# Kernel tuning notes

Hardware: AMD Instinct MI355X
Metric: run time of the kernel (lower is better)

## Reference

```python
import jax, jax.numpy as jnp
import numpy as np

BATCH, SEQ, DIM = 32, 1024, 256
CODEBOOK_SIZE = 8192
COMMITMENT_COST = 0.25
CODEBOOK_COST = 1.0


def setup_inputs() -> dict:
    key = jax.random.key(0)
    kx, kc = jax.random.split(key)
    x = jax.random.normal(kx, (BATCH, SEQ, DIM), dtype=jnp.float32)
    codebook = jax.random.normal(kc, (CODEBOOK_SIZE, DIM), dtype=jnp.float32)
    return {"x": x, "codebook": codebook, "hidden_dim": DIM}


def reference(x, codebook, hidden_dim):
    # x: [B, S, D], codebook: [K, D]
    B, S, D = x.shape
    flat = x.reshape(-1, D)  # [N, D], N = B*S
    distances = (
        jnp.sum(flat * flat, axis=1, keepdims=True)
        + jnp.sum(codebook * codebook, axis=1)
        - 2.0 * jnp.matmul(flat, codebook.T)
    )
    encoding_indices = jnp.argmin(distances, axis=1)  # [N]
    quantized = codebook[encoding_indices].reshape(x.shape)  # [B, S, D]
    # Losses (detach semantics only matter for gradients; value is same MSE)
    codebook_loss = jnp.mean((quantized - jax.lax.stop_gradient(x)) ** 2)
    commitment_loss = jnp.mean((jax.lax.stop_gradient(quantized) - x) ** 2)
    total_loss = CODEBOOK_COST * codebook_loss + COMMITMENT_COST * commitment_loss
    # Straight-through estimator
    quantized_ste = x + jax.lax.stop_gradient(quantized - x)
    return (quantized_ste, total_loss)
```

## Files before the change

kernel.cpp:

```cpp
#include <hip/hip_runtime.h>
#include <hip/hip_fp16.h>

#define NROWS 32768
#define DIMS 256
#define KCODES 8192
#define NH 2
#define HCODES 4096
#define MARGIN 0.10f

typedef _Float16 half8 __attribute__((ext_vector_type(8)));
typedef float f32x4 __attribute__((ext_vector_type(4)));
typedef unsigned long long u64;

__device__ __forceinline__ void gload_lds16(const void* g, void* l) {
  __builtin_amdgcn_global_load_lds((const __attribute__((address_space(1))) unsigned int*)g,
                                   (__attribute__((address_space(3))) unsigned int*)l, 16, 0, 0);
}

__device__ __forceinline__ unsigned sortable_f32(float f) {
  unsigned u = __float_as_uint(f);
  return u ^ (unsigned)(((int)u >> 31) | 0x80000000);
}
__device__ __forceinline__ float unsortable_f32(unsigned s) {
  const unsigned m = ((int)s < 0) ? 0x80000000u : 0xFFFFFFFFu;
  return __uint_as_float(s ^ m);
}
__device__ __forceinline__ u64 umin64(u64 a, u64 b) { return a < b ? a : b; }
__device__ __forceinline__ u64 umax64(u64 a, u64 b) { return a > b ? a : b; }
__device__ __forceinline__ float dkey(u64 k) { return unsortable_f32((unsigned)(k >> 32)); }

__global__ void k_prep(const float* __restrict__ cb, _Float16* __restrict__ cbh) {
  const int g = blockIdx.x * 256 + threadIdx.x;
  const float4 v0 = *((const float4*)cb + g * 2);
  const float4 v1 = *((const float4*)cb + g * 2 + 1);
  half8 h;
  h[0] = (_Float16)v0.x; h[1] = (_Float16)v0.y;
  h[2] = (_Float16)v0.z; h[3] = (_Float16)v0.w;
  h[4] = (_Float16)v1.x; h[5] = (_Float16)v1.y;
  h[6] = (_Float16)v1.z; h[7] = (_Float16)v1.w;
  *((half8*)cbh + g) = h;
}

__global__ void k_cnorm(const float* __restrict__ cb, float* __restrict__ cnorm,
                        int* __restrict__ wcount, int* __restrict__ scount,
                        float* __restrict__ loss_cell) {
  const int lane = threadIdx.x & 63;
  const int code = blockIdx.x * 4 + (threadIdx.x >> 6);
  const float4 v = *((const float4*)(cb + code * DIMS) + lane);
  float s = v.x * v.x + v.y * v.y + v.z * v.z + v.w * v.w;
#pragma unroll
  for (int m = 1; m < 64; m <<= 1) s += __shfl_xor(s, m);
  if (lane == 0) cnorm[code] = s;
  if (blockIdx.x == 0 && threadIdx.x == 0) {
    *wcount = 0; *scount = 0; *loss_cell = 0.0f;
  }
}

__launch_bounds__(512)
__global__ void k_gemm2(const float* __restrict__ x, const _Float16* __restrict__ cbh,
                        const float* __restrict__ cnorm,
                        u64* __restrict__ pk1, u64* __restrict__ pk2,
                        float* __restrict__ d3h) {
  __shared__ char B[2][32768];
  const int tid = threadIdx.x;
  const int lane = tid & 63;
  const int w = tid >> 6;
  const int l15 = lane & 15;
  const int lh = lane >> 4;
  const int rowblk = (int)blockIdx.x >> 1;
  const int half = (int)blockIdx.x & 1;
  const int row0 = rowblk * 256 + w * 32;
  const char* cbh_half = (const char*)(cbh + (size_t)half * HCODES * DIMS);

  half8 a[2][8];
#pragma unroll
  for (int m = 0; m < 2; ++m) {
#pragma unroll
    for (int kf = 0; kf < 8; ++kf) {
      const float* s = x + (size_t)(row0 + m * 16 + l15) * DIMS + kf * 32 + lh * 8;
      const float4 v0 = *(const float4*)s;
      const float4 v1 = *(const float4*)(s + 4);
      half8 h;
      h[0] = (_Float16)v0.x; h[1] = (_Float16)v0.y;
      h[2] = (_Float16)v0.z; h[3] = (_Float16)v0.w;
      h[4] = (_Float16)v1.x; h[5] = (_Float16)v1.y;
      h[6] = (_Float16)v1.z; h[7] = (_Float16)v1.w;
      a[m][kf] = h;
    }
  }

  int srcoff[4];
#pragma unroll
  for (int i = 0; i < 4; ++i) {
    const int L = i * 512 + tid;
    const int hi = L >> 6;
    const int lhL = hi & 3, chL = hi >> 2;
    const int code = (L & 63) ^ ((lhL & 1) << 4);
    srcoff[i] = code * 512 + chL * 64 + lhL * 16;
  }

  const int lanebase = l15 * 16 + lh * 1024;
  const int bs = (lh & 1) << 8;
  const int lbp = lanebase + bs;
  const int lbm = lanebase - bs;

  float r1[2][4], r2[2][4];
  int i1[2][4];
#pragma unroll
  for (int m = 0; m < 2; ++m)
#pragma unroll
    for (int j = 0; j < 4; ++j) { r1[m][j] = 3.0e38f; r2[m][j] = 3.0e38f; i1[m][j] = 0; }

  char* lds = &B[0][0];

  auto stage = [&](int t, int bufoff) {
#pragma unroll
    for (int i = 0; i < 4; ++i)
      gload_lds16(cbh_half + t * 32768 + srcoff[i],
                  lds + bufoff + (i * 512 + w * 64) * 16);
  };

  auto compute_tile = [&](int t, int bufoff) {
    const int cbase = half * HCODES + t * 64;
    float cn[4];
#pragma unroll
    for (int n = 0; n < 4; ++n) cn[n] = cnorm[cbase + n * 16 + l15];
    f32x4 acc[2][4];
#pragma unroll
    for (int m = 0; m < 2; ++m)
#pragma unroll
      for (int n = 0; n < 4; ++n) acc[m][n] = (f32x4){0.f, 0.f, 0.f, 0.f};
#pragma unroll
    for (int ch = 0; ch < 8; ++ch) {
      half8 b[4];
#pragma unroll
      for (int n = 0; n < 4; ++n) {
        const int ad = ((n & 1) ? lbm : lbp) + bufoff + ch * 4096 + n * 256;
        b[n] = *(const half8*)(lds + ad);
      }
#pragma unroll
      for (int m = 0; m < 2; ++m)
#pragma unroll
        for (int n = 0; n < 4; ++n)
          acc[m][n] = __builtin_amdgcn_mfma_f32_16x16x32_f16(a[m][ch], b[n], acc[m][n], 0, 0, 0);
    }
#pragma unroll
    for (int m = 0; m < 2; ++m)
#pragma unroll
      for (int n = 0; n < 4; ++n) {
        const int ic = t * 4 + n;
#pragma unroll
        for (int j = 0; j < 4; ++j) {
          const float d = fmaf(-2.0f, acc[m][n][j], cn[n]);
          const bool lt1 = d < r1[m][j];
          r2[m][j] = __builtin_amdgcn_fmed3f(d, r1[m][j], r2[m][j]);
          i1[m][j] = lt1 ? ic : i1[m][j];
          r1[m][j] = fminf(d, r1[m][j]);
        }
      }
  };

  stage(0, 0);
#pragma unroll 1
  for (int t = 0; t < 64; t += 2) {
    __syncthreads();
    if (t + 1 < 64) stage(t + 1, 32768);
    compute_tile(t, 0);
    __syncthreads();
    if (t + 2 < 64) stage(t + 2, 0);
    compute_tile(t + 1, 32768);
  }

#pragma unroll
  for (int m = 0; m < 2; ++m)
#pragma unroll
    for (int j = 0; j < 4; ++j) {
      const int ia = i1[m][j];
      const unsigned c1 = half * HCODES + (ia >> 2) * 64 + (ia & 3) * 16 + l15;
      u64 k1 = ((u64)sortable_f32(r1[m][j]) << 32) | c1;
      u64 k2 = ((u64)sortable_f32(r2[m][j]) << 32) | 0xffffffffu;
      u64 k3 = ~0ull;
#pragma unroll
      for (int mk = 1; mk < 16; mk <<= 1) {
        const u64 o1 = __shfl_xor(k1, mk);
        const u64 o2 = __shfl_xor(k2, mk);
        const u64 o3 = __shfl_xor(k3, mk);
        const u64 hi1 = umax64(k1, o1);
        k3 = umin64(umin64(k3, o3), umin64(umax64(k1, o2), umax64(k2, o1)));
        k2 = umin64(hi1, umin64(k2, o2));
        k1 = umin64(k1, o1);
      }
      if (l15 == 0) {
        const int rg = row0 + m * 16 + lh * 4 + j;
        pk1[half * NROWS + rg] = k1;
        pk2[half * NROWS + rg] = k2;
        d3h[half * NROWS + rg] = dkey(k3);
      }
    }
}

__launch_bounds__(512)
__global__ void k_gemm_fb(const float* __restrict__ x, const float* __restrict__ cb,
                          const float* __restrict__ cnorm,
                          u64* __restrict__ pk1, u64* __restrict__ pk2,
                          float* __restrict__ d3h) {
  __shared__ _Float16 clds[128][40];
  const int tid = threadIdx.x;
  const int lane = tid & 63;
  const int w = tid >> 6;
  const int l15 = lane & 15;
  const int lh = lane >> 4;
  const int rowblk = (int)blockIdx.x >> 1;
  const int half = (int)blockIdx.x & 1;
  const int row0 = rowblk * 256 + w * 32;

  half8 a[2][8];
#pragma unroll
  for (int m = 0; m < 2; ++m) {
#pragma unroll
    for (int kf = 0; kf < 8; ++kf) {
      const float* s = x + (row0 + m * 16 + l15) * DIMS + kf * 32 + lh * 8;
      const float4 v0 = *(const float4*)s;
      const float4 v1 = *(const float4*)(s + 4);
      half8 h;
      h[0] = (_Float16)v0.x; h[1] = (_Float16)v0.y;
      h[2] = (_Float16)v0.z; h[3] = (_Float16)v0.w;
      h[4] = (_Float16)v1.x; h[5] = (_Float16)v1.y;
      h[6] = (_Float16)v1.z; h[7] = (_Float16)v1.w;
      a[m][kf] = h;
    }
  }

  float r1[2][4], r2[2][4];
  int i1[2][4];
#pragma unroll
  for (int m = 0; m < 2; ++m)
#pragma unroll
    for (int j = 0; j < 4; ++j) { r1[m][j] = 3.0e38f; r2[m][j] = 3.0e38f; i1[m][j] = 0; }

  const int stg_code = tid >> 2;
  const int stg_seg = tid & 3;

  for (int ct = 0; ct < 32; ++ct) {
    const int cbase = half * HCODES + ct * 128;
    f32x4 acc[2][8];
#pragma unroll
    for (int m = 0; m < 2; ++m)
#pragma unroll
      for (int n = 0; n < 8; ++n) acc[m][n] = (f32x4){0.f, 0.f, 0.f, 0.f};

#pragma unroll
    for (int ch = 0; ch < 8; ++ch) {
      __syncthreads();
      {
        const float* s = cb + (cbase + stg_code) * DIMS + ch * 32 + stg_seg * 8;
        const float4 v0 = *(const float4*)s;
        const float4 v1 = *(const float4*)(s + 4);
        half8 h;
        h[0] = (_Float16)v0.x; h[1] = (_Float16)v0.y;
        h[2] = (_Float16)v0.z; h[3] = (_Float16)v0.w;
        h[4] = (_Float16)v1.x; h[5] = (_Float16)v1.y;
        h[6] = (_Float16)v1.z; h[7] = (_Float16)v1.w;
        *(half8*)&clds[stg_code][stg_seg * 8] = h;
      }
      __syncthreads();
      half8 b[8];
#pragma unroll
      for (int n = 0; n < 8; ++n)
        b[n] = *(const half8*)&clds[n * 16 + l15][lh * 8];
#pragma unroll
      for (int m = 0; m < 2; ++m)
#pragma unroll
        for (int n = 0; n < 8; ++n)
          acc[m][n] = __builtin_amdgcn_mfma_f32_16x16x32_f16(a[m][ch], b[n], acc[m][n], 0, 0, 0);
    }

    float cn[8];
#pragma unroll
    for (int n = 0; n < 8; ++n) cn[n] = cnorm[cbase + n * 16 + l15];
#pragma unroll
    for (int m = 0; m < 2; ++m)
#pragma unroll
      for (int n = 0; n < 8; ++n) {
        const int ic = ct * 8 + n;
#pragma unroll
        for (int j = 0; j < 4; ++j) {
          const float d = fmaf(-2.0f, acc[m][n][j], cn[n]);
          const bool lt1 = d < r1[m][j];
          r2[m][j] = __builtin_amdgcn_fmed3f(d, r1[m][j], r2[m][j]);
          i1[m][j] = lt1 ? ic : i1[m][j];
          r1[m][j] = fminf(d, r1[m][j]);
        }
      }
  }

#pragma unroll
  for (int m = 0; m < 2; ++m)
#pragma unroll
    for (int j = 0; j < 4; ++j) {
      const int ia = i1[m][j];
      const unsigned c1 = half * HCODES + (ia >> 3) * 128 + (ia & 7) * 16 + l15;
      u64 k1 = ((u64)sortable_f32(r1[m][j]) << 32) | c1;
      u64 k2 = ((u64)sortable_f32(r2[m][j]) << 32) | 0xffffffffu;
      u64 k3 = ~0ull;
#pragma unroll
      for (int mk = 1; mk < 16; mk <<= 1) {
        const u64 o1 = __shfl_xor(k1, mk);
        const u64 o2 = __shfl_xor(k2, mk);
        const u64 o3 = __shfl_xor(k3, mk);
        const u64 hi1 = umax64(k1, o1);
        k3 = umin64(umin64(k3, o3), umin64(umax64(k1, o2), umax64(k2, o1)));
        k2 = umin64(hi1, umin64(k2, o2));
        k1 = umin64(k1, o1);
      }
      if (l15 == 0) {
        const int rg = row0 + m * 16 + lh * 4 + j;
        pk1[half * NROWS + rg] = k1;
        pk2[half * NROWS + rg] = k2;
        d3h[half * NROWS + rg] = dkey(k3);
      }
    }
}

__global__ void k_merge(const u64* __restrict__ pk1, const u64* __restrict__ pk2,
                        const float* __restrict__ d3h,
                        unsigned* __restrict__ bestidx, u64* __restrict__ bestkey,
                        int* __restrict__ wlist, int* __restrict__ wcount,
                        int* __restrict__ slist, int* __restrict__ s2list,
                        int* __restrict__ scount) {
  const int r = blockIdx.x * 256 + threadIdx.x;
  const int lane = threadIdx.x & 63;
  const u64 k1a = pk1[r], k1b = pk1[NROWS + r];
  const u64 k2a = pk2[r], k2b = pk2[NROWS + r];
  const float d3a = d3h[r], d3b = d3h[NROWS + r];
  const u64 K1 = umin64(k1a, k1b);
  const u64 K2 = umin64(umax64(k1a, k1b), umin64(k2a, k2b));
  const float d3 = fminf(fminf(d3a, d3b),
                         fminf(dkey(umax64(k1a, k2b)), dkey(umax64(k2a, k1b))));
  const float d1 = dkey(K1);
  const float d2 = dkey(K2);
  const unsigned i1x = (unsigned)(K1 & 0xffffffffull);
  const unsigned i2x = (unsigned)(K2 & 0xffffffffull);
  const bool amb = (d2 - d1) < MARGIN;
  const bool hard = ((d3 - d1) < MARGIN) || (amb && i2x == 0xffffffffu);
  const bool soft = amb && !hard;
  bestidx[r] = i1x | (hard ? 0x80000000u : 0u);
  if (hard) bestkey[r] = ~0ull;
  {
    const u64 mb = __ballot(hard);
    const int cnt = __popcll(mb);
    int base = 0;
    if (lane == 0 && cnt) base = atomicAdd(wcount, cnt);
    base = __shfl(base, 0);
    if (hard) wlist[base + __popcll(mb & ((1ull << lane) - 1ull))] = r;
  }
  {
    const u64 mb = __ballot(soft);
    const int cnt = __popcll(mb);
    int base = 0;
    if (lane == 0 && cnt) base = atomicAdd(scount, cnt);
    base = __shfl(base, 0);
    if (soft) {
      const int slot = base + __popcll(mb & ((1ull << lane) - 1ull));
      slist[slot] = r;
      s2list[slot] = (int)i2x;
    }
  }
}

__launch_bounds__(256)
__global__ void k_soft(const float* __restrict__ x, const float* __restrict__ cb,
                       const int* __restrict__ slist, const int* __restrict__ s2list,
                       const int* __restrict__ scount, unsigned* __restrict__ bestidx) {
  const int tid = threadIdx.x;
  const int lane = tid & 63;
  const int gw = blockIdx.x * 4 + (tid >> 6);
  const int ns = *scount;
  for (int i = gw; i < ns; i += 256) {
    const int r = slist[i];
    const unsigned c1 = bestidx[r] & 0x7fffffffu;
    const unsigned c2 = (unsigned)s2list[i];
    const float4 xv = *((const float4*)(x + (size_t)r * DIMS) + lane);
    const float4 a = *((const float4*)(cb + (size_t)c1 * DIMS) + lane);
    const float4 b = *((const float4*)(cb + (size_t)c2 * DIMS) + lane);
    float e, p1, p2;
    e = xv.x - a.x; p1 = e * e;
    e = xv.y - a.y; p1 = fmaf(e, e, p1);
    e = xv.z - a.z; p1 = fmaf(e, e, p1);
    e = xv.w - a.w; p1 = fmaf(e, e, p1);
    e = xv.x - b.x; p2 = e * e;
    e = xv.y - b.y; p2 = fmaf(e, e, p2);
    e = xv.z - b.z; p2 = fmaf(e, e, p2);
    e = xv.w - b.w; p2 = fmaf(e, e, p2);
    double s1 = (double)p1, s2 = (double)p2;
#pragma unroll
    for (int mk = 1; mk < 64; mk <<= 1) {
      s1 += __shfl_xor(s1, mk);
      s2 += __shfl_xor(s2, mk);
    }
    unsigned win = (s1 < s2) ? c1 : ((s2 < s1) ? c2 : min(c1, c2));
    if (lane == 0) bestidx[r] = win;
  }
}

__launch_bounds__(512, 1)
__global__ void k_refine3(const float* __restrict__ x, const float* __restrict__ cb,
                          const int* __restrict__ wlist, const int* __restrict__ wcount,
                          u64* __restrict__ bestkey) {
  __shared__ float xl[2][8][272];
  __shared__ int rl[2][8];
  const int tid = threadIdx.x;
  const int lane = tid & 63;
  const int ci = tid >> 4;
  const int piece = tid & 15;
  const int codeg = blockIdx.x * 32 + ci;

  float cr[16];
  {
    const float4* cp = (const float4*)(cb + (size_t)codeg * DIMS + piece * 16);
#pragma unroll
    for (int i = 0; i < 4; ++i) {
      const float4 v = cp[i];
      cr[i * 4 + 0] = v.x; cr[i * 4 + 1] = v.y;
      cr[i * 4 + 2] = v.z; cr[i * 4 + 3] = v.w;
    }
  }

  const int nf = *wcount;
  if (nf == 0) return;
  const int nc = (nf + 7) >> 3;
  const int startc = (int)(((long long)blockIdx.x * nc) >> 8);

  const int slot = tid >> 6;
  const int dlane = tid & 63;

  auto stage = [&](int c, int buf) {
    int chunkid = startc + c;
    if (chunkid >= nc) chunkid -= nc;
    int ridx = chunkid * 8 + slot;
    if (ridx >= nf) ridx %= nf;
    const int row = wlist[ridx];
    if (dlane == 0) rl[buf][slot] = row;
    const float4* xs = (const float4*)(x + (size_t)row * DIMS) + dlane;
    *(float4*)&xl[buf][slot][dlane * 4] = *xs;
  };

  stage(0, 0);
#pragma unroll 1
  for (int c = 0; c < nc; ++c) {
    const int buf = c & 1;
    __syncthreads();
    if (c + 1 < nc) stage(c + 1, buf ^ 1);

    u64 k[8];
#pragma unroll
    for (int r = 0; r < 8; ++r) {
      const float* xr = &xl[buf][r][piece * 16];
      const float4 a0 = *(const float4*)(xr + 0);
      const float4 a1 = *(const float4*)(xr + 4);
      const float4 a2 = *(const float4*)(xr + 8);
      const float4 a3 = *(const float4*)(xr + 12);
      float s0, s1, s2, s3;
      {
        float d;
        d = a0.x - cr[0];  s0 = d * d;
        d = a0.y - cr[1];  s0 = fmaf(d, d, s0);
        d = a0.z - cr[2];  s0 = fmaf(d, d, s0);
        d = a0.w - cr[3];  s0 = fmaf(d, d, s0);
        d = a1.x - cr[4];  s1 = d * d;
        d = a1.y - cr[5];  s1 = fmaf(d, d, s1);
        d = a1.z - cr[6];  s1 = fmaf(d, d, s1);
        d = a1.w - cr[7];  s1 = fmaf(d, d, s1);
        d = a2.x - cr[8];  s2 = d * d;
        d = a2.y - cr[9];  s2 = fmaf(d, d, s2);
        d = a2.z - cr[10]; s2 = fmaf(d, d, s2);
        d = a2.w - cr[11]; s2 = fmaf(d, d, s2);
        d = a3.x - cr[12]; s3 = d * d;
        d = a3.y - cr[13]; s3 = fmaf(d, d, s3);
        d = a3.z - cr[14]; s3 = fmaf(d, d, s3);
        d = a3.w - cr[15]; s3 = fmaf(d, d, s3);
      }
      float s = (s0 + s1) + (s2 + s3);
      s += __shfl_xor(s, 1);
      s += __shfl_xor(s, 2);
      s += __shfl_xor(s, 4);
      s += __shfl_xor(s, 8);
      u64 key = ((u64)__float_as_uint(s) << 32) | (unsigned)codeg;
      u64 ok = __shfl_xor(key, 16);
      key = umin64(key, ok);
      ok = __shfl_xor(key, 32);
      key = umin64(key, ok);
      k[r] = key;
    }

    if (lane == 0) {
      int rows[8];
      u64 cur[8];
#pragma unroll
      for (int r = 0; r < 8; ++r) rows[r] = rl[buf][r];
#pragma unroll
      for (int r = 0; r < 8; ++r) cur[r] = bestkey[rows[r]];
#pragma unroll
      for (int r = 0; r < 8; ++r)
        if (k[r] < cur[r]) atomicMin(&bestkey[rows[r]], k[r]);
    }
  }
}

__launch_bounds__(256)
__global__ void k_out2(const float* __restrict__ x, const float* __restrict__ cb,
                       const unsigned* __restrict__ bestidx,
                       const u64* __restrict__ bestkey,
                       float* __restrict__ out, float* __restrict__ partials) {
  __shared__ float wsum[4];
  float s = 0.f;
#pragma unroll
  for (int it = 0; it < 4; ++it) {
    const int gid = (it * 2048 + blockIdx.x) * 256 + threadIdx.x;
    const int row = gid >> 6, d4 = gid & 63;
    const unsigned bi = bestidx[row];
    unsigned idx = bi & 0x7fffffffu;
    if (bi >> 31) idx = (unsigned)(bestkey[row] & 0xffffffffull);
    const float4 q = *(const float4*)(cb + (size_t)idx * DIMS + d4 * 4);
    const float4 xv = *(const float4*)(x + (size_t)gid * 4);
    *(float4*)(out + (size_t)gid * 4) = q;
    const float dx = q.x - xv.x, dy = q.y - xv.y, dz = q.z - xv.z, dw = q.w - xv.w;
    s += dx * dx + dy * dy + dz * dz + dw * dw;
  }
#pragma unroll
  for (int m = 1; m < 64; m <<= 1) s += __shfl_xor(s, m);
  if ((threadIdx.x & 63) == 0) wsum[threadIdx.x >> 6] = s;
  __syncthreads();
  if (threadIdx.x == 0)
    partials[blockIdx.x] = wsum[0] + wsum[1] + wsum[2] + wsum[3];
}

__global__ void k_loss(const float* __restrict__ partials, float* __restrict__ loss_cell) {
  __shared__ double wsum[4];
  double s = 0.0;
#pragma unroll
  for (int i = 0; i < 8; ++i) s += (double)partials[i * 256 + threadIdx.x];
#pragma unroll
  for (int m = 1; m < 64; m <<= 1) s += __shfl_xor(s, m);
  if ((threadIdx.x & 63) == 0) wsum[threadIdx.x >> 6] = s;
  __syncthreads();
  if (threadIdx.x == 0)
    *loss_cell = (float)((wsum[0] + wsum[1] + wsum[2] + wsum[3]) *
                         (1.25 / (double)((size_t)NROWS * DIMS)));
}

extern "C" void kernel_launch(void* const* d_in, const int* in_sizes, int n_in,
                              void* d_out, int out_size, void* d_ws, size_t ws_size,
                              hipStream_t stream) {
  const float* x = (const float*)d_in[0];
  const float* cb = (const float*)d_in[1];
  float* out = (float*)d_out;
  char* ws = (char*)d_ws;

  float* cnorm = (float*)(ws + 0);
  u64* pk1 = (u64*)(ws + 32768);
  u64* pk2 = (u64*)(ws + 557056);
  float* d3h = (float*)(ws + 1081344);
  unsigned* bestidx = (unsigned*)(ws + 1343488);
  u64* bestkey = (u64*)(ws + 1474560);
  int* wlist = (int*)(ws + 1736704);
  int* slist = (int*)(ws + 1867776);
  int* s2list = (int*)(ws + 1998848);
  int* wcount = (int*)(ws + 2129920);
  int* scount = wcount + 1;
  float* partials = (float*)(ws + 2129984);
  _Float16* cbh = (_Float16*)(ws + 2138176);
  float* loss_cell = out + (NROWS * DIMS);

  const bool fast = ws_size >= (size_t)(2138176 + KCODES * DIMS * 2);

  k_cnorm<<<KCODES / 4, 256, 0, stream>>>(cb, cnorm, wcount, scount, loss_cell);
  if (fast) {
    k_prep<<<KCODES * DIMS / 8 / 256, 256, 0, stream>>>(cb, cbh);
    k_gemm2<<<(NROWS / 256) * NH, 512, 0, stream>>>(x, cbh, cnorm, pk1, pk2, d3h);
  } else {
    k_gemm_fb<<<(NROWS / 256) * NH, 512, 0, stream>>>(x, cb, cnorm, pk1, pk2, d3h);
  }
  k_merge<<<NROWS / 256, 256, 0, stream>>>(pk1, pk2, d3h, bestidx, bestkey,
                                           wlist, wcount, slist, s2list, scount);
  k_soft<<<64, 256, 0, stream>>>(x, cb, slist, s2list, scount, bestidx);
  k_refine3<<<KCODES / 32, 512, 0, stream>>>(x, cb, wlist, wcount, bestkey);
  k_out2<<<2048, 256, 0, stream>>>(x, cb, bestidx, bestkey, out, partials);
  k_loss<<<1, 256, 0, stream>>>(partials, loss_cell);
}
```

Baseline: 225.1 us.

## Double GEMM code tile to 128 codes and fuse codebook prep with norms

The distance GEMM now stages 128 codes per tile instead of 64, with 64KB double-buffered LDS (128KB total) and 8 MFMA accumulator columns per wave. This halves the number of tile iterations and barriers and raises the MFMA work per LDS load. Separately, the fp16 codebook conversion and the code-norm computation are merged into one kernel, which saves a launch and a second read of the codebook. The larger LDS footprint and the extra accumulator registers may lower occupancy to one block per CU.

```diff
diff --git a/kernel.cpp b/kernel.cpp
--- a/kernel.cpp
+++ b/kernel.cpp
@@ -6,9 +6,11 @@
 #define KCODES 8192
 #define NH 2
 #define HCODES 4096
+#define NT 32
 #define MARGIN 0.10f
 
 typedef _Float16 half8 __attribute__((ext_vector_type(8)));
+typedef _Float16 half4 __attribute__((ext_vector_type(4)));
 typedef float f32x4 __attribute__((ext_vector_type(4)));
 typedef unsigned long long u64;
 
@@ -29,16 +31,23 @@
 __device__ __forceinline__ u64 umax64(u64 a, u64 b) { return a > b ? a : b; }
 __device__ __forceinline__ float dkey(u64 k) { return unsortable_f32((unsigned)(k >> 32)); }
 
-__global__ void k_prep(const float* __restrict__ cb, _Float16* __restrict__ cbh) {
-  const int g = blockIdx.x * 256 + threadIdx.x;
-  const float4 v0 = *((const float4*)cb + g * 2);
-  const float4 v1 = *((const float4*)cb + g * 2 + 1);
-  half8 h;
-  h[0] = (_Float16)v0.x; h[1] = (_Float16)v0.y;
-  h[2] = (_Float16)v0.z; h[3] = (_Float16)v0.w;
-  h[4] = (_Float16)v1.x; h[5] = (_Float16)v1.y;
-  h[6] = (_Float16)v1.z; h[7] = (_Float16)v1.w;
-  *((half8*)cbh + g) = h;
+__global__ void k_prep2(const float* __restrict__ cb, _Float16* __restrict__ cbh,
+                        float* __restrict__ cnorm, int* __restrict__ wcount,
+                        int* __restrict__ scount, float* __restrict__ loss_cell) {
+  const int lane = threadIdx.x & 63;
+  const int code = blockIdx.x * 4 + (threadIdx.x >> 6);
+  const float4 v = *((const float4*)(cb + (size_t)code * DIMS) + lane);
+  half4 h;
+  h[0] = (_Float16)v.x; h[1] = (_Float16)v.y;
+  h[2] = (_Float16)v.z; h[3] = (_Float16)v.w;
+  *((half4*)(cbh + (size_t)code * DIMS) + lane) = h;
+  float s = v.x * v.x + v.y * v.y + v.z * v.z + v.w * v.w;
+#pragma unroll
+  for (int m = 1; m < 64; m <<= 1) s += __shfl_xor(s, m);
+  if (lane == 0) cnorm[code] = s;
+  if (blockIdx.x == 0 && threadIdx.x == 0) {
+    *wcount = 0; *scount = 0; *loss_cell = 0.0f;
+  }
 }
 
 __global__ void k_cnorm(const float* __restrict__ cb, float* __restrict__ cnorm,
@@ -61,7 +70,7 @@
                         const float* __restrict__ cnorm,
                         u64* __restrict__ pk1, u64* __restrict__ pk2,
                         float* __restrict__ d3h) {
-  __shared__ char B[2][32768];
+  __shared__ char B[2][65536];
   const int tid = threadIdx.x;
   const int lane = tid & 63;
   const int w = tid >> 6;
@@ -89,17 +98,17 @@
     }
   }
 
-  int srcoff[4];
-#pragma unroll
-  for (int i = 0; i < 4; ++i) {
+  int srcoff[8];
+#pragma unroll
+  for (int i = 0; i < 8; ++i) {
     const int L = i * 512 + tid;
-    const int hi = L >> 6;
+    const int hi = L >> 7;
     const int lhL = hi & 3, chL = hi >> 2;
-    const int code = (L & 63) ^ ((lhL & 1) << 4);
+    const int code = (L & 127) ^ ((lhL & 1) << 4);
     srcoff[i] = code * 512 + chL * 64 + lhL * 16;
   }
 
-  const int lanebase = l15 * 16 + lh * 1024;
+  const int lanebase = l15 * 16 + lh * 2048;
   const int bs = (lh & 1) << 8;
   const int lbp = lanebase + bs;
   const int lbm = lanebase - bs;
@@ -115,40 +124,40 @@
 
   auto stage = [&](int t, int bufoff) {
 #pragma unroll
-    for (int i = 0; i < 4; ++i)
-      gload_lds16(cbh_half + t * 32768 + srcoff[i],
+    for (int i = 0; i < 8; ++i)
+      gload_lds16(cbh_half + t * 65536 + srcoff[i],
                   lds + bufoff + (i * 512 + w * 64) * 16);
   };
 
   auto compute_tile = [&](int t, int bufoff) {
-    const int cbase = half * HCODES + t * 64;
-    float cn[4];
-#pragma unroll
-    for (int n = 0; n < 4; ++n) cn[n] = cnorm[cbase + n * 16 + l15];
-    f32x4 acc[2][4];
+    const int cbase = half * HCODES + t * 128;
+    float cn[8];
+#pragma unroll
+    for (int n = 0; n < 8; ++n) cn[n] = cnorm[cbase + n * 16 + l15];
+    f32x4 acc[2][8];
 #pragma unroll
     for (int m = 0; m < 2; ++m)
 #pragma unroll
-      for (int n = 0; n < 4; ++n) acc[m][n] = (f32x4){0.f, 0.f, 0.f, 0.f};
+      for (int n = 0; n < 8; ++n) acc[m][n] = (f32x4){0.f, 0.f, 0.f, 0.f};
 #pragma unroll
     for (int ch = 0; ch < 8; ++ch) {
-      half8 b[4];
-#pragma unroll
-      for (int n = 0; n < 4; ++n) {
-        const int ad = ((n & 1) ? lbm : lbp) + bufoff + ch * 4096 + n * 256;
+      half8 b[8];
+#pragma unroll
+      for (int n = 0; n < 8; ++n) {
+        const int ad = ((n & 1) ? lbm : lbp) + bufoff + ch * 8192 + n * 256;
         b[n] = *(const half8*)(lds + ad);
       }
 #pragma unroll
       for (int m = 0; m < 2; ++m)
 #pragma unroll
-        for (int n = 0; n < 4; ++n)
+        for (int n = 0; n < 8; ++n)
           acc[m][n] = __builtin_amdgcn_mfma_f32_16x16x32_f16(a[m][ch], b[n], acc[m][n], 0, 0, 0);
     }
 #pragma unroll
     for (int m = 0; m < 2; ++m)
 #pragma unroll
-      for (int n = 0; n < 4; ++n) {
-        const int ic = t * 4 + n;
+      for (int n = 0; n < 8; ++n) {
+        const int ic = t * 8 + n;
 #pragma unroll
         for (int j = 0; j < 4; ++j) {
           const float d = fmaf(-2.0f, acc[m][n][j], cn[n]);
@@ -162,13 +171,13 @@
 
   stage(0, 0);
 #pragma unroll 1
-  for (int t = 0; t < 64; t += 2) {
+  for (int t = 0; t < NT; t += 2) {
     __syncthreads();
-    if (t + 1 < 64) stage(t + 1, 32768);
+    if (t + 1 < NT) stage(t + 1, 65536);
     compute_tile(t, 0);
     __syncthreads();
-    if (t + 2 < 64) stage(t + 2, 0);
-    compute_tile(t + 1, 32768);
+    if (t + 2 < NT) stage(t + 2, 0);
+    compute_tile(t + 1, 65536);
   }
 
 #pragma unroll
@@ -176,7 +185,7 @@
 #pragma unroll
     for (int j = 0; j < 4; ++j) {
       const int ia = i1[m][j];
-      const unsigned c1 = half * HCODES + (ia >> 2) * 64 + (ia & 3) * 16 + l15;
+      const unsigned c1 = half * HCODES + (ia >> 3) * 128 + (ia & 7) * 16 + l15;
       u64 k1 = ((u64)sortable_f32(r1[m][j]) << 32) | c1;
       u64 k2 = ((u64)sortable_f32(r2[m][j]) << 32) | 0xffffffffu;
       u64 k3 = ~0ull;
@@ -574,11 +583,11 @@
 
   const bool fast = ws_size >= (size_t)(2138176 + KCODES * DIMS * 2);
 
-  k_cnorm<<<KCODES / 4, 256, 0, stream>>>(cb, cnorm, wcount, scount, loss_cell);
   if (fast) {
-    k_prep<<<KCODES * DIMS / 8 / 256, 256, 0, stream>>>(cb, cbh);
+    k_prep2<<<KCODES / 4, 256, 0, stream>>>(cb, cbh, cnorm, wcount, scount, loss_cell);
     k_gemm2<<<(NROWS / 256) * NH, 512, 0, stream>>>(x, cbh, cnorm, pk1, pk2, d3h);
   } else {
+    k_cnorm<<<KCODES / 4, 256, 0, stream>>>(cb, cnorm, wcount, scount, loss_cell);
     k_gemm_fb<<<(NROWS / 256) * NH, 512, 0, stream>>>(x, cb, cnorm, pk1, pk2, d3h);
   }
   k_merge<<<NROWS / 256, 256, 0, stream>>>(pk1, pk2, d3h, bestidx, bestkey,
```

Measured after the change: 232.3 us. 1.03x slower.
